# Performance work log

Measured on AMD Instinct MI355X. Metric: run time of the kernel, lower is better.

The kernel has to match this reference:

```python
import jax, jax.numpy as jnp
import numpy as np

WS = 10
NUM_HEADS = 12
DIM = 384


def setup_inputs() -> dict:
    key = jax.random.key(0)
    k1, k2, k3 = jax.random.split(key, 3)
    B, t, H, W, C = 2, 4, 44, 44, DIM
    x = jax.random.normal(k1, (B * t, H * W, C), dtype=jnp.float32)
    qkv_w = jax.random.normal(k2, (3 * C, C), dtype=jnp.float32) * 0.02
    proj_w = jax.random.normal(k3, (C, C), dtype=jnp.float32) * 0.02
    proj_b = jnp.zeros((C,), dtype=jnp.float32)
    return {"x": x, "qkv_w": qkv_w, "proj_w": proj_w, "proj_b": proj_b,
            "t": t, "H": H, "W": W}


def reference(x, qkv_w, proj_w, proj_b, t, H, W):
    ws, nh = WS, NUM_HEADS
    BT, N, C = x.shape
    B = BT // t
    hd = C // nh
    scale = hd ** (-0.5)

    ax = x.reshape(B, t, H, W, C)
    pad_r = (ws - W % ws) % ws
    pad_b = (ws - H % ws) % ws
    if pad_r > 0 or pad_b > 0:
        ax = jnp.pad(ax, ((0, 0), (0, 0), (0, pad_b), (0, pad_r), (0, 0)))
    hg, wg = (H + ws - 1) // ws, (W + ws - 1) // ws
    # partition into windows: each window holds t*ws*ws tokens
    ax = ax.reshape(B, t, hg, ws, wg, ws, C)
    ax = ax.transpose(0, 2, 4, 1, 3, 5, 6).reshape(B, hg * wg, t * ws * ws, C)

    qkv = ax @ qkv_w.T  # (B, nw, n, 3C)
    qkv = qkv.reshape(B, hg * wg, t * ws * ws, 3, nh, hd)
    qkv = qkv.transpose(3, 0, 1, 4, 2, 5)  # (3, B, nw, nh, n, hd)
    q, k, v = qkv[0], qkv[1], qkv[2]

    attn = jnp.einsum('bwhnd,bwhmd->bwhnm', q, k) * scale
    attn = jax.nn.softmax(attn, axis=-1)
    out = jnp.einsum('bwhnm,bwhmd->bwhnd', attn, v)  # (B, nw, nh, n, hd)
    out = out.transpose(0, 1, 3, 2, 4).reshape(B, hg * wg, t * ws * ws, C)

    # reverse window partition
    out = out.reshape(B, hg, wg, t, ws, ws, C)
    out = out.transpose(0, 3, 1, 4, 2, 5, 6).reshape(B, t, hg * ws, wg * ws, C)
    out = out[:, :, :H, :W, :]
    out = out.reshape(B, t * H * W, C)
    out = out @ proj_w.T + proj_b
    return out.reshape(-1, N, C)
```

## Files before the change

kernel.cpp:

```cpp
#include <hip/hip_runtime.h>
#include <cstddef>

typedef __attribute__((ext_vector_type(8))) short bf16x8;
typedef __attribute__((ext_vector_type(4))) float f32x4;
typedef __attribute__((ext_vector_type(16))) float f32x16;
typedef unsigned short ushort_t;

namespace {
constexpr int Tt = 4, Hh = 44, Ww = 44, Cc = 384, NH = 12, HD = 32;
constexpr int NWIN = 25, NT = 400, NTP = 416, NPOS = Hh * Ww;
constexpr int NTOK = 2 * Tt * NPOS;
constexpr float SCALE = 0.17677669529663687f;
constexpr float LOG2E = 1.4426950408889634f;
constexpr size_t XN  = (size_t)NTOK * Cc;
constexpr size_t WN  = (size_t)3 * Cc * Cc;
constexpr size_t PWN = (size_t)Cc * Cc;
constexpr size_t PLN = (size_t)600 * NTP * HD;
}

__device__ __forceinline__ ushort_t f2bf(float f) {
  unsigned u = __builtin_bit_cast(unsigned, f);
  u += 0x7fffu + ((u >> 16) & 1u);
  return (ushort_t)(u >> 16);
}

__device__ __forceinline__ unsigned cvt_pk_bf16(float a, float b) {
  unsigned r;
  asm volatile("v_cvt_pk_bf16_f32 %0, %1, %2" : "=v"(r) : "v"(a), "v"(b));
  return r;
}

__device__ __forceinline__ void gload16(const void* g, void* l) {
  __builtin_amdgcn_global_load_lds(
      (const __attribute__((address_space(1))) unsigned int*)g,
      (__attribute__((address_space(3))) unsigned int*)l, 16, 0, 0);
}

__global__ __launch_bounds__(256) void conv_all(
    const float* __restrict__ x, const float* __restrict__ w1,
    const float* __restrict__ w2, ushort_t* __restrict__ xo,
    ushort_t* __restrict__ w1o, ushort_t* __restrict__ w2o,
    ushort_t* __restrict__ kpl, ushort_t* __restrict__ vpl) {
  constexpr int XN8 = (int)(XN / 8), WN8 = (int)(WN / 8), PN8 = (int)(PWN / 8);
  constexpr int TOT8 = XN8 + WN8 + PN8;
  constexpr int ZTOT = 50 * NTP * NH;
  const int i = blockIdx.x * 256 + threadIdx.x;
  if (i < TOT8) {
    const float* s;
    ushort_t* d;
    int j;
    if (i < XN8)            { s = x;  d = xo;  j = i; }
    else if (i < XN8 + WN8) { s = w1; d = w1o; j = i - XN8; }
    else                    { s = w2; d = w2o; j = i - XN8 - WN8; }
    const float4* s4 = (const float4*)s;
    float4 a = s4[2 * j], bq = s4[2 * j + 1];
    union { bf16x8 v; ushort_t u[8]; } o;
    o.u[0] = f2bf(a.x);  o.u[1] = f2bf(a.y);  o.u[2] = f2bf(a.z);  o.u[3] = f2bf(a.w);
    o.u[4] = f2bf(bq.x); o.u[5] = f2bf(bq.y); o.u[6] = f2bf(bq.z); o.u[7] = f2bf(bq.w);
    ((bf16x8*)d)[j] = o.v;
  } else if (i < TOT8 + ZTOT) {
    const int j = i - TOT8;
    const int pair = j / NH, head = j - pair * NH;
    const int bw = pair / NTP, kk = pair - bw * NTP;
    const int win = bw % NWIN, hi5 = win / 5, wi5 = win % 5;
    bool fill;
    if (kk >= NT) {
      fill = true;
    } else {
      const int rem = kk % 100;
      const int hh = rem / 10, ww2 = rem - hh * 10;
      fill = (hi5 == 4 && hh >= 4) || (wi5 == 4 && ww2 >= 4);
    }
    if (fill) {
      const size_t off = ((size_t)(bw * NH + head) * NTP + kk) * HD;
      bf16x8 z;
      z[0]=0;z[1]=0;z[2]=0;z[3]=0;z[4]=0;z[5]=0;z[6]=0;z[7]=0;
#pragma unroll
      for (int p = 0; p < 4; ++p) {
        ((bf16x8*)(kpl + off))[p] = z;
        ((bf16x8*)(vpl + off))[p] = z;
      }
    }
  }
}

__global__ __launch_bounds__(256) void qkv_mfma(
    const ushort_t* __restrict__ xb, const ushort_t* __restrict__ wb,
    ushort_t* __restrict__ qpl, ushort_t* __restrict__ kpl,
    ushort_t* __restrict__ vpl) {
  __shared__ __align__(16) unsigned char As[8192];
  __shared__ __align__(16) unsigned char Bs[8192];
  const unsigned bid = blockIdx.x;
  const unsigned xcd = bid & 7u, slot = bid >> 3;
  const unsigned wgid = (xcd == 0 ? 0u : 137u + (xcd - 1u) * 136u) + slot;
  const int nt = wgid % 9, mt = wgid / 9;
  const int tid = threadIdx.x, lane = tid & 63, wid = tid >> 6;
  const int wm = wid >> 1, wn = wid & 1;
  const int g = lane >> 4, q = lane & 15;
  const int m0 = mt * 128, n0 = nt * 128;

  const unsigned char* xB = (const unsigned char*)xb;
  const unsigned char* wB = (const unsigned char*)wb;

  size_t aoff[2], boff[2];
  unsigned ldsoff[2];
#pragma unroll
  for (int p = 0; p < 2; ++p) {
    const int row = wid * 32 + p * 16 + (lane >> 2);
    const int gs = (lane & 3) ^ ((row >> 1) & 3);
    aoff[p] = (size_t)(m0 + row) * 768 + gs * 16;
    boff[p] = (size_t)(n0 + row) * 768 + gs * 16;
    ldsoff[p] = wid * 2048 + p * 1024;
  }

  f32x4 acc[4][4] = {};

  for (int kb = 0; kb < 12; ++kb) {
    if (kb) __syncthreads();
#pragma unroll
    for (int p = 0; p < 2; ++p) {
      gload16(xB + aoff[p] + kb * 64, As + ldsoff[p]);
      gload16(wB + boff[p] + kb * 64, Bs + ldsoff[p]);
    }
    __syncthreads();
    bf16x8 tfr[4], wfr[4];
#pragma unroll
    for (int i = 0; i < 4; ++i) {
      const int ar = wm * 64 + i * 16 + q;
      tfr[i] = *(const bf16x8*)(As + ar * 64 + ((g ^ ((ar >> 1) & 3)) << 4));
      const int br = wn * 64 + i * 16 + q;
      wfr[i] = *(const bf16x8*)(Bs + br * 64 + ((g ^ ((br >> 1) & 3)) << 4));
    }
#pragma unroll
    for (int i = 0; i < 4; ++i)
#pragma unroll
      for (int j = 0; j < 4; ++j)
        acc[i][j] = __builtin_amdgcn_mfma_f32_16x16x32_bf16(wfr[i], tfr[j],
                                                            acc[i][j], 0, 0, 0);
  }

  const float QS = SCALE * LOG2E;
#pragma unroll
  for (int j = 0; j < 4; ++j) {
    const int t = m0 + wm * 64 + j * 16 + q;
    const int bt = t / NPOS, pos = t - bt * NPOS;
    const int h = pos / Ww, w = pos - h * Ww;
    const int b = bt >> 2, tt = bt & 3;
    const int hq = h / 10, wq = w / 10;
    const int kk = tt * 100 + (h - hq * 10) * 10 + (w - wq * 10);
    const int bw = b * NWIN + hq * 5 + wq;
#pragma unroll
    for (int i = 0; i < 4; ++i) {
      const int col = n0 + wn * 64 + i * 16 + 4 * g;
      const int which = col / Cc;
      const int head = (col - which * Cc) >> 5;
      const int d4 = col & 31;
      ushort_t* pl = which == 0 ? qpl : (which == 1 ? kpl : vpl);
      const float scl = which == 0 ? QS : 1.0f;
      uint2 st;
      st.x = cvt_pk_bf16(acc[i][j][0] * scl, acc[i][j][1] * scl);
      st.y = cvt_pk_bf16(acc[i][j][2] * scl, acc[i][j][3] * scl);
      *(uint2*)(pl + ((size_t)(bw * NH + head) * NTP + kk) * HD + d4) = st;
    }
  }
}

__global__ __launch_bounds__(448) void attn_mfma(
    const ushort_t* __restrict__ qpl, const ushort_t* __restrict__ kpl,
    const ushort_t* __restrict__ vpl, ushort_t* __restrict__ aout) {
  __shared__ __align__(16) unsigned char Vt[32 * 896];

  const int wh = blockIdx.x;
  const int head = wh % NH, bw = wh / NH;
  const int b = bw / NWIN, win = bw % NWIN, hi5 = win / 5, wi5 = win % 5;

  const int tid = threadIdx.x, lane = tid & 63, wid = tid >> 6;
  const int l31 = lane & 31, hi = lane >> 5;

  const ushort_t* qbase = qpl + (size_t)wh * (NTP * HD);
  const ushort_t* kbase = kpl + (size_t)wh * (NTP * HD);
  const ushort_t* vbase = vpl + (size_t)wh * (NTP * HD);

  for (int slot = tid; slot < 1664; slot += 448) {
    const int key = slot >> 2, dblk = (slot & 3) * 8;
    union { bf16x8 v; ushort_t u[8]; } t;
    t.v = *(const bf16x8*)(vbase + (size_t)key * HD + dblk);
    const int kc = key >> 3, klo = key & 7;
#pragma unroll
    for (int j = 0; j < 8; ++j) {
      const int d = dblk + j;
      const int f = (d & 7) ^ ((d >> 3) & 3);
      *(ushort_t*)(Vt + d * 896 + ((kc ^ f) << 4) + klo * 2) = t.u[j];
    }
  }
  __syncthreads();

  const int fv = (l31 & 7) ^ ((l31 >> 3) & 3);
  const unsigned char* vrow = Vt + l31 * 896;

  for (int tile = wid; tile < 13; tile += 7) {
    const int qrow = tile * 32 + l31;
    const ushort_t* qp = qbase + (size_t)qrow * HD;
    const bf16x8 qfa = *(const bf16x8*)(qp + hi * 8);
    const bf16x8 qfb = *(const bf16x8*)(qp + 16 + hi * 8);

    unsigned koff = (unsigned)l31 * HD;
    bf16x8 kf0 = *(const bf16x8*)(kbase + koff + hi * 8);
    bf16x8 kf1 = *(const bf16x8*)(kbase + koff + 16 + hi * 8);

    f32x16 o = {};
    float lpart = 0.f;

    for (int c = 0; c < 13; ++c) {
      f32x16 s = {};
      __builtin_amdgcn_s_setprio(1);
      s = __builtin_amdgcn_mfma_f32_32x32x16_bf16(kf0, qfa, s, 0, 0, 0);
      s = __builtin_amdgcn_mfma_f32_32x32x16_bf16(kf1, qfb, s, 0, 0, 0);
      __builtin_amdgcn_s_setprio(0);

      if (c < 12) {
        koff += 32u * HD;
        kf0 = *(const bf16x8*)(kbase + koff + hi * 8);
        kf1 = *(const bf16x8*)(kbase + koff + 16 + hi * 8);
      }

      if (c == 12) {
#pragma unroll
        for (int r = 8; r < 16; ++r) s[r] = -1e30f;
      }

      float e[16];
#pragma unroll
      for (int r = 0; r < 16; ++r) e[r] = __builtin_amdgcn_exp2f(s[r]);
      lpart += ((e[0] + e[1]) + (e[2] + e[3])) + ((e[4] + e[5]) + (e[6] + e[7])) +
               (((e[8] + e[9]) + (e[10] + e[11])) +
                ((e[12] + e[13]) + (e[14] + e[15])));

      unsigned w0 = cvt_pk_bf16(e[0], e[1]),   w1 = cvt_pk_bf16(e[2], e[3]);
      unsigned w2 = cvt_pk_bf16(e[4], e[5]),   w3 = cvt_pk_bf16(e[6], e[7]);
      unsigned w4 = cvt_pk_bf16(e[8], e[9]),   w5 = cvt_pk_bf16(e[10], e[11]);
      unsigned w6 = cvt_pk_bf16(e[12], e[13]), w7 = cvt_pk_bf16(e[14], e[15]);
      asm volatile("v_permlane32_swap_b32 %0, %1" : "+v"(w0), "+v"(w2));
      asm volatile("v_permlane32_swap_b32 %0, %1" : "+v"(w1), "+v"(w3));
      asm volatile("v_permlane32_swap_b32 %0, %1" : "+v"(w4), "+v"(w6));
      asm volatile("v_permlane32_swap_b32 %0, %1" : "+v"(w5), "+v"(w7));
      union { bf16x8 v; unsigned u[4]; } p0, p1;
      p0.u[0] = w0; p0.u[1] = w1; p0.u[2] = w2; p0.u[3] = w3;
      p1.u[0] = w4; p1.u[1] = w5; p1.u[2] = w6; p1.u[3] = w7;

      const bf16x8 vf0 = *(const bf16x8*)(vrow + (((4 * c + hi) ^ fv) << 4));
      const bf16x8 vf1 = *(const bf16x8*)(vrow + (((4 * c + 2 + hi) ^ fv) << 4));
      __builtin_amdgcn_s_setprio(1);
      o = __builtin_amdgcn_mfma_f32_32x32x16_bf16(vf0, p0.v, o, 0, 0, 0);
      o = __builtin_amdgcn_mfma_f32_32x32x16_bf16(vf1, p1.v, o, 0, 0, 0);
      __builtin_amdgcn_s_setprio(0);
    }

    lpart += __shfl_xor(lpart, 32);

    {
      const int tt = qrow / 100, rem = qrow - tt * 100;
      const int hh = rem / 10, ww2 = rem - hh * 10;
      const int h = hi5 * 10 + hh, w = wi5 * 10 + ww2;
      if (qrow < NT && h < Hh && w < Ww) {
        const int qtok = (b * Tt + tt) * NPOS + h * Ww + w;
        ushort_t* dst = aout + (size_t)qtok * Cc + head * HD;
        const float inv = 1.0f / lpart;
#pragma unroll
        for (int g4 = 0; g4 < 4; ++g4) {
          unsigned lo  = cvt_pk_bf16(o[4 * g4 + 0] * inv, o[4 * g4 + 1] * inv);
          unsigned hi2 = cvt_pk_bf16(o[4 * g4 + 2] * inv, o[4 * g4 + 3] * inv);
          uint2 st; st.x = lo; st.y = hi2;
          *(uint2*)(dst + 8 * g4 + 4 * hi) = st;
        }
      }
    }
  }
}

__global__ __launch_bounds__(256) void proj_mfma(
    const ushort_t* __restrict__ ab, const ushort_t* __restrict__ pw,
    const float* __restrict__ bias, float* __restrict__ out) {
  __shared__ __align__(16) unsigned char As[8192];
  __shared__ __align__(16) unsigned char Bs[8192];
  const int nt = blockIdx.x, mt = blockIdx.y;
  const int tid = threadIdx.x, lane = tid & 63, wid = tid >> 6;
  const int wm = wid >> 1, wn = wid & 1;
  const int g = lane >> 4, q = lane & 15;
  const int m0 = mt * 128, n0 = nt * 128;

  const unsigned char* aB = (const unsigned char*)ab;
  const unsigned char* wB = (const unsigned char*)pw;

  size_t aoff[2], boff[2];
  unsigned ldsoff[2];
#pragma unroll
  for (int p = 0; p < 2; ++p) {
    const int row = wid * 32 + p * 16 + (lane >> 2);
    const int gs = (lane & 3) ^ ((row >> 1) & 3);
    aoff[p] = (size_t)(m0 + row) * 768 + gs * 16;
    boff[p] = (size_t)(n0 + row) * 768 + gs * 16;
    ldsoff[p] = wid * 2048 + p * 1024;
  }

  f32x4 acc[4][4] = {};

  for (int kb = 0; kb < 12; ++kb) {
    if (kb) __syncthreads();
#pragma unroll
    for (int p = 0; p < 2; ++p) {
      gload16(aB + aoff[p] + kb * 64, As + ldsoff[p]);
      gload16(wB + boff[p] + kb * 64, Bs + ldsoff[p]);
    }
    __syncthreads();
    bf16x8 tfr[4], wfr[4];
#pragma unroll
    for (int i = 0; i < 4; ++i) {
      const int ar = wm * 64 + i * 16 + q;
      tfr[i] = *(const bf16x8*)(As + ar * 64 + ((g ^ ((ar >> 1) & 3)) << 4));
      const int br = wn * 64 + i * 16 + q;
      wfr[i] = *(const bf16x8*)(Bs + br * 64 + ((g ^ ((br >> 1) & 3)) << 4));
    }
#pragma unroll
    for (int i = 0; i < 4; ++i)
#pragma unroll
      for (int j = 0; j < 4; ++j)
        acc[i][j] = __builtin_amdgcn_mfma_f32_16x16x32_bf16(wfr[i], tfr[j],
                                                            acc[i][j], 0, 0, 0);
  }

#pragma unroll
  for (int j = 0; j < 4; ++j) {
    const int t = m0 + wm * 64 + j * 16 + q;
#pragma unroll
    for (int i = 0; i < 4; ++i) {
      const int col = n0 + wn * 64 + i * 16 + 4 * g;
      const float4 bb = *(const float4*)(bias + col);
      float4 st;
      st.x = acc[i][j][0] + bb.x;
      st.y = acc[i][j][1] + bb.y;
      st.z = acc[i][j][2] + bb.z;
      st.w = acc[i][j][3] + bb.w;
      *(float4*)(out + (size_t)t * Cc + col) = st;
    }
  }
}

extern "C" void kernel_launch(void* const* d_in, const int* in_sizes, int n_in,
                              void* d_out, int out_size, void* d_ws,
                              size_t ws_size, hipStream_t stream) {
  const float* x      = (const float*)d_in[0];
  const float* qkv_w  = (const float*)d_in[1];
  const float* proj_w = (const float*)d_in[2];
  const float* proj_b = (const float*)d_in[3];

  ushort_t* xb    = (ushort_t*)d_ws;
  ushort_t* wb    = xb + XN;
  ushort_t* pwb   = wb + WN;
  ushort_t* qpl   = pwb + PWN;
  ushort_t* kpl   = qpl + PLN;
  ushort_t* vpl   = kpl + PLN;
  ushort_t* attnb = vpl + PLN;

  constexpr int TOT8 = (int)((XN + WN + PWN) / 8);
  constexpr int ZTOT = 50 * NTP * NH;
  conv_all<<<(TOT8 + ZTOT + 255) / 256, 256, 0, stream>>>(
      x, qkv_w, proj_w, xb, wb, pwb, kpl, vpl);
  qkv_mfma<<<1089, 256, 0, stream>>>(xb, wb, qpl, kpl, vpl);
  attn_mfma<<<600, 448, 0, stream>>>(qpl, kpl, vpl, attnb);
  proj_mfma<<<dim3(3, 121), 256, 0, stream>>>(attnb, pwb, proj_b, (float*)d_out);
}
```

Before: 87.99 us.

## Fuse fp32-to-bf16 conversion of activations into the QKV GEMM load path

Removes the separate pass that converted the full fp32 activation tensor to bf16 in workspace. The QKV GEMM now reads fp32 x directly, converts in registers with packed bf16 conversion, and writes swizzled tiles into LDS. This avoids an extra write and read of the activation tensor. In exchange, the A operand loses its async global-to-LDS path and x is read at twice the bytes, and each x element is re-read by the 9 N-tile blocks. The weight conversion also switches to the packed conversion instruction.

```diff
diff --git a/kernel.cpp b/kernel.cpp
--- a/kernel.cpp
+++ b/kernel.cpp
@@ -12,16 +12,9 @@
 constexpr int NTOK = 2 * Tt * NPOS;
 constexpr float SCALE = 0.17677669529663687f;
 constexpr float LOG2E = 1.4426950408889634f;
-constexpr size_t XN  = (size_t)NTOK * Cc;
 constexpr size_t WN  = (size_t)3 * Cc * Cc;
 constexpr size_t PWN = (size_t)Cc * Cc;
 constexpr size_t PLN = (size_t)600 * NTP * HD;
-}
-
-__device__ __forceinline__ ushort_t f2bf(float f) {
-  unsigned u = __builtin_bit_cast(unsigned, f);
-  u += 0x7fffu + ((u >> 16) & 1u);
-  return (ushort_t)(u >> 16);
 }
 
 __device__ __forceinline__ unsigned cvt_pk_bf16(float a, float b) {
@@ -36,27 +29,25 @@
       (__attribute__((address_space(3))) unsigned int*)l, 16, 0, 0);
 }
 
-__global__ __launch_bounds__(256) void conv_all(
-    const float* __restrict__ x, const float* __restrict__ w1,
-    const float* __restrict__ w2, ushort_t* __restrict__ xo,
+__global__ __launch_bounds__(256) void conv_wz(
+    const float* __restrict__ w1, const float* __restrict__ w2,
     ushort_t* __restrict__ w1o, ushort_t* __restrict__ w2o,
     ushort_t* __restrict__ kpl, ushort_t* __restrict__ vpl) {
-  constexpr int XN8 = (int)(XN / 8), WN8 = (int)(WN / 8), PN8 = (int)(PWN / 8);
-  constexpr int TOT8 = XN8 + WN8 + PN8;
+  constexpr int WN8 = (int)(WN / 8), PN8 = (int)(PWN / 8);
+  constexpr int TOT8 = WN8 + PN8;
   constexpr int ZTOT = 50 * NTP * NH;
   const int i = blockIdx.x * 256 + threadIdx.x;
   if (i < TOT8) {
     const float* s;
     ushort_t* d;
     int j;
-    if (i < XN8)            { s = x;  d = xo;  j = i; }
-    else if (i < XN8 + WN8) { s = w1; d = w1o; j = i - XN8; }
-    else                    { s = w2; d = w2o; j = i - XN8 - WN8; }
+    if (i < WN8) { s = w1; d = w1o; j = i; }
+    else         { s = w2; d = w2o; j = i - WN8; }
     const float4* s4 = (const float4*)s;
     float4 a = s4[2 * j], bq = s4[2 * j + 1];
-    union { bf16x8 v; ushort_t u[8]; } o;
-    o.u[0] = f2bf(a.x);  o.u[1] = f2bf(a.y);  o.u[2] = f2bf(a.z);  o.u[3] = f2bf(a.w);
-    o.u[4] = f2bf(bq.x); o.u[5] = f2bf(bq.y); o.u[6] = f2bf(bq.z); o.u[7] = f2bf(bq.w);
+    union { bf16x8 v; unsigned u[4]; } o;
+    o.u[0] = cvt_pk_bf16(a.x, a.y);   o.u[1] = cvt_pk_bf16(a.z, a.w);
+    o.u[2] = cvt_pk_bf16(bq.x, bq.y); o.u[3] = cvt_pk_bf16(bq.z, bq.w);
     ((bf16x8*)d)[j] = o.v;
   } else if (i < TOT8 + ZTOT) {
     const int j = i - TOT8;
@@ -85,7 +76,7 @@
 }
 
 __global__ __launch_bounds__(256) void qkv_mfma(
-    const ushort_t* __restrict__ xb, const ushort_t* __restrict__ wb,
+    const float* __restrict__ xf, const ushort_t* __restrict__ wb,
     ushort_t* __restrict__ qpl, ushort_t* __restrict__ kpl,
     ushort_t* __restrict__ vpl) {
   __shared__ __align__(16) unsigned char As[8192];
@@ -99,16 +90,19 @@
   const int g = lane >> 4, q = lane & 15;
   const int m0 = mt * 128, n0 = nt * 128;
 
-  const unsigned char* xB = (const unsigned char*)xb;
   const unsigned char* wB = (const unsigned char*)wb;
 
-  size_t aoff[2], boff[2];
+  const float* xp[2];
+  unsigned xlds[2];
+  size_t boff[2];
   unsigned ldsoff[2];
 #pragma unroll
   for (int p = 0; p < 2; ++p) {
     const int row = wid * 32 + p * 16 + (lane >> 2);
-    const int gs = (lane & 3) ^ ((row >> 1) & 3);
-    aoff[p] = (size_t)(m0 + row) * 768 + gs * 16;
+    const int ch = lane & 3;
+    xp[p] = xf + (size_t)(m0 + row) * Cc + ch * 8;
+    xlds[p] = row * 64 + (((ch ^ (row >> 1)) & 3) << 4);
+    const int gs = ch ^ ((row >> 1) & 3);
     boff[p] = (size_t)(n0 + row) * 768 + gs * 16;
     ldsoff[p] = wid * 2048 + p * 1024;
   }
@@ -118,9 +112,16 @@
   for (int kb = 0; kb < 12; ++kb) {
     if (kb) __syncthreads();
 #pragma unroll
+    for (int p = 0; p < 2; ++p)
+      gload16(wB + boff[p] + kb * 64, Bs + ldsoff[p]);
+#pragma unroll
     for (int p = 0; p < 2; ++p) {
-      gload16(xB + aoff[p] + kb * 64, As + ldsoff[p]);
-      gload16(wB + boff[p] + kb * 64, Bs + ldsoff[p]);
+      const float4 a = *(const float4*)(xp[p] + kb * 32);
+      const float4 b = *(const float4*)(xp[p] + kb * 32 + 4);
+      union { bf16x8 v; unsigned u[4]; } t;
+      t.u[0] = cvt_pk_bf16(a.x, a.y); t.u[1] = cvt_pk_bf16(a.z, a.w);
+      t.u[2] = cvt_pk_bf16(b.x, b.y); t.u[3] = cvt_pk_bf16(b.z, b.w);
+      *(bf16x8*)(As + xlds[p]) = t.v;
     }
     __syncthreads();
     bf16x8 tfr[4], wfr[4];
@@ -354,19 +355,18 @@
   const float* proj_w = (const float*)d_in[2];
   const float* proj_b = (const float*)d_in[3];
 
-  ushort_t* xb    = (ushort_t*)d_ws;
-  ushort_t* wb    = xb + XN;
+  ushort_t* wb    = (ushort_t*)d_ws;
   ushort_t* pwb   = wb + WN;
   ushort_t* qpl   = pwb + PWN;
   ushort_t* kpl   = qpl + PLN;
   ushort_t* vpl   = kpl + PLN;
   ushort_t* attnb = vpl + PLN;
 
-  constexpr int TOT8 = (int)((XN + WN + PWN) / 8);
+  constexpr int TOT8 = (int)((WN + PWN) / 8);
   constexpr int ZTOT = 50 * NTP * NH;
-  conv_all<<<(TOT8 + ZTOT + 255) / 256, 256, 0, stream>>>(
-      x, qkv_w, proj_w, xb, wb, pwb, kpl, vpl);
-  qkv_mfma<<<1089, 256, 0, stream>>>(xb, wb, qpl, kpl, vpl);
+  conv_wz<<<(TOT8 + ZTOT + 255) / 256, 256, 0, stream>>>(qkv_w, proj_w, wb,
+                                                         pwb, kpl, vpl);
+  qkv_mfma<<<1089, 256, 0, stream>>>(x, wb, qpl, kpl, vpl);
   attn_mfma<<<600, 448, 0, stream>>>(qpl, kpl, vpl, attnb);
   proj_mfma<<<dim3(3, 121), 256, 0, stream>>>(attnb, pwb, proj_b, (float*)d_out);
 }
```

Measured after the change: 92.34 us. 1.05x slower.
